# Performance work log

Measured on AMD Instinct MI355X. Metric: run time of the kernel, lower is better.

## Reference

```python
import jax, jax.numpy as jnp
import numpy as np

ALPHA_LO = float(np.exp(-1.0 / 5.0))   # 0.81873...
ALPHA_HI = float(np.exp(-1.0 / 25.0))  # 0.96079...
T_CROP = 0


def setup_inputs() -> dict:
    key = jax.random.key(0)
    k1, k2, k3, k4 = jax.random.split(key, 4)
    B, T, I, H = 64, 2000, 512, 512
    x = jax.random.normal(k1, (B, T, I), dtype=jnp.float32)
    # W ~ U(-sqrt(1/I), sqrt(1/I)) per nn.init.uniform_
    lim = float(np.sqrt(1.0 / I))
    W = jax.random.uniform(k2, (H, I), dtype=jnp.float32, minval=-lim, maxval=lim)
    # alpha ~ U(alpha_lim[0], alpha_lim[1])
    alpha = jax.random.uniform(k3, (H,), dtype=jnp.float32, minval=ALPHA_LO, maxval=ALPHA_HI)
    # initial membrane potential ~ U(0,1) (torch.rand in _readout_cell)
    u0 = jax.random.uniform(k4, (B, H), dtype=jnp.float32)
    return {"x": x, "W": W, "alpha": alpha, "u0": u0}


def reference(x, W, alpha, u0):
    # x: [B, T, I], W: [H, I] -> Wx: [B, T, H]
    alpha_c = jnp.clip(alpha, ALPHA_LO, ALPHA_HI)  # [H]
    beta = 1.0 - alpha_c                           # [H]
    Wx = jnp.einsum("bti,hi->bth", x, W)          # [B, T, H]
    Wx_t = jnp.swapaxes(Wx, 0, 1)                  # [T, B, H] for scan

    out0 = jnp.zeros_like(u0)

    def step(carry, inp):
        ut, out, t = carry
        wx_t = inp  # [B, H]
        ut = alpha_c * ut + beta * wx_t
        out = out + jnp.where(t >= T_CROP, jax.nn.softmax(ut, axis=1), 0.0)
        return (ut, out, t + 1), None

    (_, out, _), _ = jax.lax.scan(step, (u0, out0, jnp.int32(0)), Wx_t)
    return out  # [B, H]
```

## Files before the change

### kernel.cpp

```cpp
#include <hip/hip_runtime.h>
#include <hip/hip_bf16.h>
#include <stdint.h>

#define ALPHA_LO 0.8187307530779818f
#define ALPHA_HI 0.9607894391523232f

#define BATCH 64
#define TT    2000
#define II    512
#define HH    512
#define MM    (BATCH*TT)
#define LCH   50
#define CCH   (TT/LCH)

typedef __bf16 bf16;
typedef bf16  bf16x8 __attribute__((ext_vector_type(8)));
typedef bf16  bf16x4 __attribute__((ext_vector_type(4)));
typedef float f32x4  __attribute__((ext_vector_type(4)));

__global__ void k_convW(const float* __restrict__ W, bf16* __restrict__ Wbt) {
    const int t  = blockIdx.x * 256 + threadIdx.x;
    const int h  = t >> 6;
    const int kb = t & 63;
    const float* src = W + (size_t)h * II + kb * 8;
    float4 v0 = *(const float4*)(src);
    float4 v1 = *(const float4*)(src + 4);
    bf16x8 o;
    o[0]=(bf16)v0.x; o[1]=(bf16)v0.y; o[2]=(bf16)v0.z; o[3]=(bf16)v0.w;
    o[4]=(bf16)v1.x; o[5]=(bf16)v1.y; o[6]=(bf16)v1.z; o[7]=(bf16)v1.w;
    const int ntile = h >> 8, r = h & 255, k0 = kb >> 2, kq = kb & 3;
    bf16* dst = Wbt + (size_t)ntile * 131072 + k0 * 8192 + kq * 2048 + r * 8;
    *(bf16x8*)dst = o;
}

__global__ __launch_bounds__(256, 2) void k_gemm(const float* __restrict__ X,
                                                 const bf16* __restrict__ Wbt,
                                                 bf16* __restrict__ Y) {
    __shared__ bf16 Al[4 * 128 * 8];
    __shared__ bf16 Bl[4 * 256 * 8];
    const int tid  = threadIdx.x;
    const int bx   = blockIdx.x;
    const int m0   = (bx >> 1) * 128;
    const int nt   = bx & 1;
    const int lane = tid & 63;
    const int wv   = tid >> 6;
    const int wr   = (wv >> 1) * 64;
    const int wc   = (wv & 1) * 128;
    const int fr   = lane & 15;
    const int kq   = lane >> 4;

    f32x4 acc[4][8] = {};

    const int ar  = tid >> 1;
    const int acq = tid & 1;
    const float* xa = X + (size_t)(m0 + ar) * II + acq * 16;
    bf16* aw0 = &Al[(acq * 2) * 1024 + ar * 8];
    bf16* aw1 = aw0 + 1024;

    const bf16* wsrc = Wbt + (size_t)nt * 131072 + wv * 512 + lane * 8;

    float4 av[4];
    #pragma unroll
    for (int q = 0; q < 4; ++q) av[q] = *(const float4*)(xa + q * 4);

    for (int ks = 0; ks < 16; ++ks) {
        __syncthreads();
        bf16x8 c0, c1;
        c0[0]=(bf16)av[0].x; c0[1]=(bf16)av[0].y; c0[2]=(bf16)av[0].z; c0[3]=(bf16)av[0].w;
        c0[4]=(bf16)av[1].x; c0[5]=(bf16)av[1].y; c0[6]=(bf16)av[1].z; c0[7]=(bf16)av[1].w;
        c1[0]=(bf16)av[2].x; c1[1]=(bf16)av[2].y; c1[2]=(bf16)av[2].z; c1[3]=(bf16)av[2].w;
        c1[4]=(bf16)av[3].x; c1[5]=(bf16)av[3].y; c1[6]=(bf16)av[3].z; c1[7]=(bf16)av[3].w;
        *(bf16x8*)aw0 = c0;
        *(bf16x8*)aw1 = c1;
        #pragma unroll
        for (int q = 0; q < 4; ++q)
            __builtin_amdgcn_global_load_lds(
                (const __attribute__((address_space(1))) unsigned int*)(wsrc + (size_t)ks * 8192 + q * 2048),
                (__attribute__((address_space(3))) unsigned int*)(&Bl[q * 2048 + wv * 512]),
                16, 0, 0);
        if (ks < 15) {
            #pragma unroll
            for (int q = 0; q < 4; ++q)
                av[q] = *(const float4*)(xa + (ks + 1) * 32 + q * 4);
        }
        __syncthreads();

        bf16x8 af[4], bfr[8];
        #pragma unroll
        for (int i = 0; i < 4; ++i)
            af[i] = *(const bf16x8*)(&Al[kq * 1024 + (wr + i * 16 + fr) * 8]);
        #pragma unroll
        for (int j = 0; j < 8; ++j)
            bfr[j] = *(const bf16x8*)(&Bl[kq * 2048 + (wc + j * 16 + fr) * 8]);
        #pragma unroll
        for (int i = 0; i < 4; ++i)
            #pragma unroll
            for (int j = 0; j < 8; ++j)
                acc[i][j] = __builtin_amdgcn_mfma_f32_16x16x32_bf16(af[i], bfr[j], acc[i][j], 0, 0, 0);
    }

    const int n0 = nt * 256;
    #pragma unroll
    for (int i = 0; i < 4; ++i)
        #pragma unroll
        for (int j = 0; j < 8; ++j) {
            const int row = m0 + wr + i * 16 + kq * 4;
            const int col = n0 + wc + j * 16 + fr;
            #pragma unroll
            for (int r = 0; r < 4; ++r)
                Y[(size_t)(row + r) * HH + col] = (bf16)acc[i][j][r];
        }
}

__global__ void k_chunk(const bf16* __restrict__ Y, const float* __restrict__ alpha,
                        float* __restrict__ P) {
    const int c = blockIdx.x, b = blockIdx.y;
    const int lane = threadIdx.x;
    const int h0 = lane * 8;
    float a[8], p[8];
    #pragma unroll
    for (int k = 0; k < 8; ++k) {
        a[k] = fminf(fmaxf(alpha[h0 + k], ALPHA_LO), ALPHA_HI);
        p[k] = 0.f;
    }
    const bf16* base = Y + ((size_t)b * TT + (size_t)c * LCH) * HH + h0;
    for (int j = 0; j < LCH; ++j) {
        bf16x8 w = *(const bf16x8*)(base + (size_t)j * HH);
        #pragma unroll
        for (int k = 0; k < 8; ++k) p[k] = a[k] * p[k] + (float)w[k];
    }
    float* po = P + ((size_t)c * BATCH + b) * HH + h0;
    #pragma unroll
    for (int k = 0; k < 8; ++k) po[k] = (1.f - a[k]) * p[k];
}

__global__ void k_prefix(const float* __restrict__ alpha, const float* __restrict__ u0,
                         const float* __restrict__ P, float* __restrict__ V) {
    const int g = blockIdx.x * 256 + threadIdx.x;
    const int h = g & (HH - 1);
    float a = fminf(fmaxf(alpha[h], ALPHA_LO), ALPHA_HI);
    float a2 = a * a, a4 = a2 * a2, a5 = a4 * a;
    float b2 = a5 * a5, b4 = b2 * b2, a25 = b4 * a5;
    float aL = a25 * a25;
    float v = u0[g];
    for (int c = 0; c < CCH; ++c) {
        const size_t idx = (size_t)c * (BATCH * HH) + g;
        V[idx] = v;
        v = aL * v + P[idx];
    }
}

__global__ void k_soft(const bf16* __restrict__ Y, const float* __restrict__ alpha,
                       const float* __restrict__ V, float* __restrict__ OutP) {
    const int c = blockIdx.x, b = blockIdx.y;
    const int lane = threadIdx.x;
    const int h0 = lane * 8;
    float a[8], bt[8], u[8], o[8];
    #pragma unroll
    for (int k = 0; k < 8; ++k) {
        a[k]  = fminf(fmaxf(alpha[h0 + k], ALPHA_LO), ALPHA_HI);
        bt[k] = 1.f - a[k];
        o[k]  = 0.f;
    }
    const float* vb = V + ((size_t)c * BATCH + b) * HH + h0;
    #pragma unroll
    for (int k = 0; k < 8; ++k) u[k] = vb[k];
    const bf16* base = Y + ((size_t)b * TT + (size_t)c * LCH) * HH + h0;
    for (int j = 0; j < LCH; ++j) {
        bf16x8 w = *(const bf16x8*)(base + (size_t)j * HH);
        float e[8], s = 0.f;
        #pragma unroll
        for (int k = 0; k < 8; ++k) {
            u[k] = a[k] * u[k] + bt[k] * (float)w[k];
            e[k] = __expf(u[k]);
            s += e[k];
        }
        #pragma unroll
        for (int off = 32; off >= 1; off >>= 1) s += __shfl_xor(s, off, 64);
        const float inv = 1.f / s;
        #pragma unroll
        for (int k = 0; k < 8; ++k) o[k] += e[k] * inv;
    }
    float* po = OutP + ((size_t)c * BATCH + b) * HH + h0;
    #pragma unroll
    for (int k = 0; k < 8; ++k) po[k] = o[k];
}

__global__ void k_reduce(const float* __restrict__ OutP, float* __restrict__ out) {
    const int g = blockIdx.x * 256 + threadIdx.x;
    float s = 0.f;
    for (int c = 0; c < CCH; ++c) s += OutP[(size_t)c * (BATCH * HH) + g];
    out[g] = s;
}

extern "C" void kernel_launch(void* const* d_in, const int* in_sizes, int n_in,
                              void* d_out, int out_size, void* d_ws, size_t ws_size,
                              hipStream_t stream) {
    const float* x     = (const float*)d_in[0];
    const float* W     = (const float*)d_in[1];
    const float* alpha = (const float*)d_in[2];
    const float* u0    = (const float*)d_in[3];
    float* out = (float*)d_out;

    char* ws = (char*)d_ws;
    bf16* Wbt = (bf16*)ws;
    bf16* Yx  = (bf16*)(ws + 524288);
    float* P  = (float*)(ws + 524288 + 131072000);
    float* V  = P + (size_t)CCH * BATCH * HH;
    float* OutP = V + (size_t)CCH * BATCH * HH;

    hipLaunchKernelGGL(k_convW,  dim3(128),               dim3(256), 0, stream, W, Wbt);
    hipLaunchKernelGGL(k_gemm,   dim3((MM/128) * 2),      dim3(256), 0, stream, x, Wbt, Yx);
    hipLaunchKernelGGL(k_chunk,  dim3(CCH, BATCH),        dim3(64),  0, stream, Yx, alpha, P);
    hipLaunchKernelGGL(k_prefix, dim3(BATCH*HH/256),      dim3(256), 0, stream, alpha, u0, P, V);
    hipLaunchKernelGGL(k_soft,   dim3(CCH, BATCH),        dim3(64),  0, stream, Yx, alpha, V, OutP);
    hipLaunchKernelGGL(k_reduce, dim3(BATCH*HH/256),      dim3(256), 0, stream, OutP, out);
}
```

Before: 204.6 us.

## Restructure GEMM to full-N tiles with multi-stage LDS pipeline and single barrier

The GEMM now uses 512-thread blocks that each compute a full 128x512 output tile, so every X row block is read and converted to bf16 only once instead of twice. W is re-laid out so each k-step slice is contiguous, and it is prefetched two steps ahead into a 4-deep LDS ring, with the A tile double-buffered. This replaces two barriers per step with one and raises MFMA priority. The cost is much larger LDS use (about 136 KB per block), which may cap occupancy at one block per CU. Correctness of the single-barrier ring depends on the buffer distances being large enough.

New measurement: 176.1 us. -13.9%, faster.

```diff
diff --git a/kernel.cpp b/kernel.cpp
--- a/kernel.cpp
+++ b/kernel.cpp
@@ -15,8 +15,11 @@
 
 typedef __bf16 bf16;
 typedef bf16  bf16x8 __attribute__((ext_vector_type(8)));
-typedef bf16  bf16x4 __attribute__((ext_vector_type(4)));
 typedef float f32x4  __attribute__((ext_vector_type(4)));
+
+#define GLDS(src, dst) __builtin_amdgcn_global_load_lds( \
+    (const __attribute__((address_space(1))) unsigned int*)(src), \
+    (__attribute__((address_space(3))) unsigned int*)(dst), 16, 0, 0)
 
 __global__ void k_convW(const float* __restrict__ W, bf16* __restrict__ Wbt) {
     const int t  = blockIdx.x * 256 + threadIdx.x;
@@ -28,84 +31,87 @@
     bf16x8 o;
     o[0]=(bf16)v0.x; o[1]=(bf16)v0.y; o[2]=(bf16)v0.z; o[3]=(bf16)v0.w;
     o[4]=(bf16)v1.x; o[5]=(bf16)v1.y; o[6]=(bf16)v1.z; o[7]=(bf16)v1.w;
-    const int ntile = h >> 8, r = h & 255, k0 = kb >> 2, kq = kb & 3;
-    bf16* dst = Wbt + (size_t)ntile * 131072 + k0 * 8192 + kq * 2048 + r * 8;
+    bf16* dst = Wbt + (size_t)(kb >> 2) * 16384 + h * 32 + (kb & 3) * 8;
     *(bf16x8*)dst = o;
 }
 
-__global__ __launch_bounds__(256, 2) void k_gemm(const float* __restrict__ X,
+__global__ __launch_bounds__(512, 2) void k_gemm(const float* __restrict__ X,
                                                  const bf16* __restrict__ Wbt,
                                                  bf16* __restrict__ Y) {
-    __shared__ bf16 Al[4 * 128 * 8];
-    __shared__ bf16 Bl[4 * 256 * 8];
+    __shared__ bf16 Al[2][128 * 32];
+    __shared__ bf16 Bl[4][512 * 32];
     const int tid  = threadIdx.x;
-    const int bx   = blockIdx.x;
-    const int m0   = (bx >> 1) * 128;
-    const int nt   = bx & 1;
+    const int m0   = blockIdx.x * 128;
     const int lane = tid & 63;
     const int wv   = tid >> 6;
-    const int wr   = (wv >> 1) * 64;
-    const int wc   = (wv & 1) * 128;
+    const int wr   = (wv >> 2) * 64;
+    const int wc   = (wv & 3) * 128;
     const int fr   = lane & 15;
     const int kq   = lane >> 4;
 
     f32x4 acc[4][8] = {};
 
-    const int ar  = tid >> 1;
-    const int acq = tid & 1;
-    const float* xa = X + (size_t)(m0 + ar) * II + acq * 16;
-    bf16* aw0 = &Al[(acq * 2) * 1024 + ar * 8];
-    bf16* aw1 = aw0 + 1024;
-
-    const bf16* wsrc = Wbt + (size_t)nt * 131072 + wv * 512 + lane * 8;
-
-    float4 av[4];
-    #pragma unroll
-    for (int q = 0; q < 4; ++q) av[q] = *(const float4*)(xa + q * 4);
-
+    const int ar   = tid >> 2;
+    const int ak   = (tid & 3) * 8;
+    const int aoff = ar * 32 + ak;
+    const float* xa = X + (size_t)(m0 + ar) * II + ak;
+
+    const bf16* wsrc = Wbt + wv * 512 + lane * 8;
+
+    float4 av[3][2];
+
+    #pragma unroll
+    for (int q = 0; q < 4; ++q) GLDS(wsrc + q * 4096,         &Bl[0][(q * 8 + wv) * 512]);
+    av[0][0] = *(const float4*)(xa);
+    av[0][1] = *(const float4*)(xa + 4);
+    #pragma unroll
+    for (int q = 0; q < 4; ++q) GLDS(wsrc + 16384 + q * 4096, &Bl[1][(q * 8 + wv) * 512]);
+    av[1][0] = *(const float4*)(xa + 32);
+    av[1][1] = *(const float4*)(xa + 36);
+
+    #pragma unroll
     for (int ks = 0; ks < 16; ++ks) {
-        __syncthreads();
-        bf16x8 c0, c1;
-        c0[0]=(bf16)av[0].x; c0[1]=(bf16)av[0].y; c0[2]=(bf16)av[0].z; c0[3]=(bf16)av[0].w;
-        c0[4]=(bf16)av[1].x; c0[5]=(bf16)av[1].y; c0[6]=(bf16)av[1].z; c0[7]=(bf16)av[1].w;
-        c1[0]=(bf16)av[2].x; c1[1]=(bf16)av[2].y; c1[2]=(bf16)av[2].z; c1[3]=(bf16)av[2].w;
-        c1[4]=(bf16)av[3].x; c1[5]=(bf16)av[3].y; c1[6]=(bf16)av[3].z; c1[7]=(bf16)av[3].w;
-        *(bf16x8*)aw0 = c0;
-        *(bf16x8*)aw1 = c1;
-        #pragma unroll
-        for (int q = 0; q < 4; ++q)
-            __builtin_amdgcn_global_load_lds(
-                (const __attribute__((address_space(1))) unsigned int*)(wsrc + (size_t)ks * 8192 + q * 2048),
-                (__attribute__((address_space(3))) unsigned int*)(&Bl[q * 2048 + wv * 512]),
-                16, 0, 0);
-        if (ks < 15) {
+        const int bcur = ks & 3;
+        const int acur = ks & 1;
+        const int rcur = ks % 3;
+        if (ks + 2 < 16) {
             #pragma unroll
             for (int q = 0; q < 4; ++q)
-                av[q] = *(const float4*)(xa + (ks + 1) * 32 + q * 4);
+                GLDS(wsrc + (size_t)(ks + 2) * 16384 + q * 4096,
+                     &Bl[(ks + 2) & 3][(q * 8 + wv) * 512]);
+            av[(ks + 2) % 3][0] = *(const float4*)(xa + (size_t)(ks + 2) * 32);
+            av[(ks + 2) % 3][1] = *(const float4*)(xa + (size_t)(ks + 2) * 32 + 4);
         }
-        __syncthreads();
-
-        bf16x8 af[4], bfr[8];
+        float4 a0 = av[rcur][0], a1 = av[rcur][1];
+        bf16x8 c;
+        c[0]=(bf16)a0.x; c[1]=(bf16)a0.y; c[2]=(bf16)a0.z; c[3]=(bf16)a0.w;
+        c[4]=(bf16)a1.x; c[5]=(bf16)a1.y; c[6]=(bf16)a1.z; c[7]=(bf16)a1.w;
+        *(bf16x8*)(&Al[acur][aoff]) = c;
+        asm volatile("s_waitcnt lgkmcnt(0)" ::: "memory");
+        __builtin_amdgcn_s_barrier();
+        bf16x8 af[4], bb[8];
         #pragma unroll
         for (int i = 0; i < 4; ++i)
-            af[i] = *(const bf16x8*)(&Al[kq * 1024 + (wr + i * 16 + fr) * 8]);
+            af[i] = *(const bf16x8*)(&Al[acur][(wr + i * 16 + fr) * 32 + kq * 8]);
         #pragma unroll
         for (int j = 0; j < 8; ++j)
-            bfr[j] = *(const bf16x8*)(&Bl[kq * 2048 + (wc + j * 16 + fr) * 8]);
+            bb[j] = *(const bf16x8*)(&Bl[bcur][(wc + j * 16 + fr) * 32 + kq * 8]);
+        __builtin_amdgcn_s_setprio(1);
         #pragma unroll
         for (int i = 0; i < 4; ++i)
             #pragma unroll
             for (int j = 0; j < 8; ++j)
-                acc[i][j] = __builtin_amdgcn_mfma_f32_16x16x32_bf16(af[i], bfr[j], acc[i][j], 0, 0, 0);
-    }
-
-    const int n0 = nt * 256;
+                acc[i][j] = __builtin_amdgcn_mfma_f32_16x16x32_bf16(af[i], bb[j], acc[i][j], 0, 0, 0);
+        __builtin_amdgcn_s_setprio(0);
+        asm volatile("" ::: "memory");
+    }
+
     #pragma unroll
     for (int i = 0; i < 4; ++i)
         #pragma unroll
         for (int j = 0; j < 8; ++j) {
             const int row = m0 + wr + i * 16 + kq * 4;
-            const int col = n0 + wc + j * 16 + fr;
+            const int col = wc + j * 16 + fr;
             #pragma unroll
             for (int r = 0; r < 4; ++r)
                 Y[(size_t)(row + r) * HH + col] = (bf16)acc[i][j][r];
@@ -209,10 +215,10 @@
     float* V  = P + (size_t)CCH * BATCH * HH;
     float* OutP = V + (size_t)CCH * BATCH * HH;
 
-    hipLaunchKernelGGL(k_convW,  dim3(128),               dim3(256), 0, stream, W, Wbt);
-    hipLaunchKernelGGL(k_gemm,   dim3((MM/128) * 2),      dim3(256), 0, stream, x, Wbt, Yx);
-    hipLaunchKernelGGL(k_chunk,  dim3(CCH, BATCH),        dim3(64),  0, stream, Yx, alpha, P);
-    hipLaunchKernelGGL(k_prefix, dim3(BATCH*HH/256),      dim3(256), 0, stream, alpha, u0, P, V);
-    hipLaunchKernelGGL(k_soft,   dim3(CCH, BATCH),        dim3(64),  0, stream, Yx, alpha, V, OutP);
-    hipLaunchKernelGGL(k_reduce, dim3(BATCH*HH/256),      dim3(256), 0, stream, OutP, out);
-}
+    hipLaunchKernelGGL(k_convW,  dim3(128),          dim3(256), 0, stream, W, Wbt);
+    hipLaunchKernelGGL(k_gemm,   dim3(MM / 128),     dim3(512), 0, stream, x, Wbt, Yx);
+    hipLaunchKernelGGL(k_chunk,  dim3(CCH, BATCH),   dim3(64),  0, stream, Yx, alpha, P);
+    hipLaunchKernelGGL(k_prefix, dim3(BATCH*HH/256), dim3(256), 0, stream, alpha, u0, P, V);
+    hipLaunchKernelGGL(k_soft,   dim3(CCH, BATCH),   dim3(64),  0, stream, Yx, alpha, V, OutP);
+    hipLaunchKernelGGL(k_reduce, dim3(BATCH*HH/256), dim3(256), 0, stream, OutP, out);
+}
```
